# Optimization experiments

Hardware: AMD Instinct MI355X
Metric: run time of the kernel (lower is better)

The kernel has to match this reference:

```python
import jax, jax.numpy as jnp
import numpy as np

D = 1024
NH = 16
HD = D // NH          # 64
GRID = 24             # sqrt(N) for 2D RoPE
HID = 4 * D           # SwiGLU hidden
SOFT_CAP = 50.0
EPS = 1e-6


def _rms(x, g):
    return x * jax.lax.rsqrt(jnp.mean(x * x, axis=-1, keepdims=True) + EPS) * g


def _rotate_half(x):
    h = x.shape[-1] // 2
    return jnp.concatenate([-x[..., h:], x[..., :h]], axis=-1)


def _rope2d_tables():
    half = HD // 2                                   # 32 dims per build, tiled to 64
    inv_freq = 1.0 / (10000.0 ** (jnp.arange(0, half, 2, dtype=jnp.float32) / half))  # (16,)
    idx = jnp.arange(GRID * GRID)
    pr = (idx // GRID).astype(jnp.float32)
    pc = (idx % GRID).astype(jnp.float32)
    freqs = jnp.concatenate([pr[:, None] * inv_freq, pc[:, None] * inv_freq], axis=-1)  # (N,32)
    cos = jnp.concatenate([jnp.cos(freqs), jnp.cos(freqs)], axis=-1)  # (N,64)
    sin = jnp.concatenate([jnp.sin(freqs), jnp.sin(freqs)], axis=-1)
    return cos, sin


def setup_inputs() -> dict:
    key = jax.random.key(0)
    ks = jax.random.split(key, 14)
    B, T, N = 1, 16, GRID * GRID
    s = 0.02
    return {
        "x": jax.random.normal(ks[0], (B, T, N, D), jnp.float32),
        "wq": jax.random.normal(ks[1], (D, D), jnp.float32) * s,
        "wk": jax.random.normal(ks[2], (D, D), jnp.float32) * s,
        "wv": jax.random.normal(ks[3], (D, D), jnp.float32) * s,
        "wo": jax.random.normal(ks[4], (D, D), jnp.float32) * s,
        "gq": jnp.ones((HD,), jnp.float32),
        "gk": jnp.ones((HD,), jnp.float32),
        "g1": jnp.ones((D,), jnp.float32),
        "g2": jnp.ones((D,), jnp.float32),
        "w1": jax.random.normal(ks[5], (D, HID), jnp.float32) * s,
        "w3": jax.random.normal(ks[6], (D, HID), jnp.float32) * s,
        "w2": jax.random.normal(ks[7], (HID, D), jnp.float32) * s,
        "space_mask": jnp.ones((N, N), bool),
        "rope_indices": jnp.arange(N, dtype=jnp.int32),
        "T": 16,
    }


def reference(x, wq, wk, wv, wo, gq, gk, g1, g2, w1, w3, w2, space_mask, rope_indices, T):
    B, T_, N, _ = x.shape
    BT = B * T_
    xs = x.reshape(BT, N, D)

    # --- spatial attention with pre-RMSNorm ---
    h = _rms(xs, g1)
    q = (h @ wq).reshape(BT, N, NH, HD).transpose(0, 2, 1, 3)  # (BT,H,N,hd)
    k = (h @ wk).reshape(BT, N, NH, HD).transpose(0, 2, 1, 3)
    v = (h @ wv).reshape(BT, N, NH, HD).transpose(0, 2, 1, 3)

    # QKNorm: RMSNorm over head_dim with learned scale
    q = q * jax.lax.rsqrt(jnp.mean(q * q, axis=-1, keepdims=True) + EPS) * gq
    k = k * jax.lax.rsqrt(jnp.mean(k * k, axis=-1, keepdims=True) + EPS) * gk

    # 2D RoPE gathered by rope_indices, masked by valid (>=0) indices
    cos, sin = _rope2d_tables()
    safe = jnp.clip(rope_indices, 0, None)
    cos_sel = cos[safe][None, None]  # (1,1,N,hd)
    sin_sel = sin[safe][None, None]
    valid = (rope_indices >= 0)[None, None, :, None]
    q = jnp.where(valid, q * cos_sel + _rotate_half(q) * sin_sel, q)
    k = jnp.where(valid, k * cos_sel + _rotate_half(k) * sin_sel, k)

    scale = HD ** -0.5
    attn = jnp.einsum('bhqd,bhkd->bhqk', q, k) * scale
    attn = SOFT_CAP * jnp.tanh(attn / SOFT_CAP)                 # soft cap
    attn = jnp.where(space_mask[None, None], attn, -jnp.inf)
    attn = jax.nn.softmax(attn.astype(jnp.float32), axis=-1).astype(v.dtype)
    out = jnp.einsum('bhqk,bhkd->bhqd', attn, v)
    out = out.transpose(0, 2, 1, 3).reshape(BT, N, D) @ wo
    xs = xs + out

    # --- SwiGLU FFN with pre-RMSNorm ---
    h2 = _rms(xs, g2)
    ff = (jax.nn.silu(h2 @ w1) * (h2 @ w3)) @ w2
    xs = xs + ff

    return xs.reshape(B, T_, N, D)
```

## Files before the change

### kernel.cpp

```cpp
#include <hip/hip_runtime.h>
#include <hip/hip_bf16.h>


#define D_    1024
#define NH_   16
#define HD_   64
#define NT_   576
#define ROWS_ 9216
#define HID_  4096

typedef __attribute__((ext_vector_type(8))) short bf16x8;
typedef __attribute__((ext_vector_type(4))) float f32x4;

__device__ __forceinline__ unsigned short f2bf(float f) {
  union { float f; unsigned int u; } v; v.f = f;
  unsigned int r = v.u + 0x7FFFu + ((v.u >> 16) & 1u);
  return (unsigned short)(r >> 16);
}
__device__ __forceinline__ float bf2f(unsigned short u) {
  union { unsigned int u; float f; } v; v.u = ((unsigned int)u) << 16;
  return v.f;
}

#define MFMA(a, b, c) __builtin_amdgcn_mfma_f32_16x16x32_bf16((a), (b), (c), 0, 0, 0)

#define GLOAD16(gptr, lptr)                                                        \
  __builtin_amdgcn_global_load_lds(                                                \
      (const __attribute__((address_space(1))) void*)(gptr),                       \
      (__attribute__((address_space(3))) void*)(lptr), 16, 0, 0)

__global__ __launch_bounds__(256) void transpose_w(
    const float* __restrict__ W, unsigned short* __restrict__ Wt, int K, int N) {
  __shared__ float tile[64][65];
  int n0 = blockIdx.x * 64, k0 = blockIdx.y * 64;
  int t = threadIdx.x, c = t & 63, r0 = t >> 6;
#pragma unroll
  for (int i = 0; i < 16; ++i) {
    int r = r0 + i * 4;
    tile[r][c] = W[(size_t)(k0 + r) * N + n0 + c];
  }
  __syncthreads();
#pragma unroll
  for (int i = 0; i < 16; ++i) {
    int r = r0 + i * 4;
    Wt[(size_t)(n0 + r) * K + k0 + c] = f2bf(tile[c][r]);
  }
}

__global__ void rope_tables(float* __restrict__ cosT, float* __restrict__ sinT) {
  int n = blockIdx.x, d = threadIdx.x;
  float pr = (float)(n / 24), pc = (float)(n % 24);
  int fi = d & 31, j = fi & 15;
  float pos = (fi < 16) ? pr : pc;
  float invf = powf(10000.0f, -(float)j * (1.0f / 16.0f));
  float f = pos * invf;
  cosT[n * 64 + d] = cosf(f);
  sinT[n * 64 + d] = sinf(f);
}

__global__ __launch_bounds__(256) void rmsnorm_bf16(
    const float* __restrict__ X, const float* __restrict__ g,
    unsigned short* __restrict__ O) {
  int row = blockIdx.x, t = threadIdx.x;
  const float4 v = ((const float4*)(X + (size_t)row * D_))[t];
  float ss = v.x * v.x + v.y * v.y + v.z * v.z + v.w * v.w;
#pragma unroll
  for (int o = 32; o; o >>= 1) ss += __shfl_xor(ss, o);
  __shared__ float red[4];
  if ((t & 63) == 0) red[t >> 6] = ss;
  __syncthreads();
  float tot = red[0] + red[1] + red[2] + red[3];
  float r = rsqrtf(tot * (1.0f / D_) + 1e-6f);
  const float4 gv = ((const float4*)g)[t];
  ushort4 pack = make_ushort4(f2bf(v.x * r * gv.x), f2bf(v.y * r * gv.y),
                              f2bf(v.z * r * gv.z), f2bf(v.w * r * gv.w));
  ((ushort4*)(O + (size_t)row * D_))[t] = pack;
}

template <int MODE, int BN>
__global__ __launch_bounds__(256) void gemm_bf16(
    const unsigned short* __restrict__ A, const unsigned short* __restrict__ Bt,
    void* __restrict__ Cout, const float* __restrict__ R,
    unsigned short* __restrict__ q_out, unsigned short* __restrict__ k_out,
    unsigned short* __restrict__ v_out, int M, int N, int K) {
  constexpr int NREP = BN / 32;
  __shared__ unsigned short lA[128 * 32];
  __shared__ unsigned short lB[BN * 32];
  const int t = threadIdx.x;
  const int w = t >> 6, l = t & 63;
  const int fr = l & 15, fq = l >> 4;
  const int m0 = blockIdx.y * 128, n0 = blockIdx.x * BN;
  const int wm = (w >> 1) * 64, wn = (w & 1) * (BN / 2);

  f32x4 acc[4][NREP] = {};

  for (int k0 = 0; k0 < K; k0 += 32) {
#pragma unroll
    for (int c = 0; c < 2; ++c) {
      int f = t * 16 + c * 4096;
      GLOAD16(A + (size_t)(m0 + (f >> 6)) * K + k0 + ((f & 63) >> 1),
              (char*)lA + f);
    }
#pragma unroll
    for (int c = 0; c < BN / 64; ++c) {
      int f = t * 16 + c * 4096;
      GLOAD16(Bt + (size_t)(n0 + (f >> 6)) * K + k0 + ((f & 63) >> 1),
              (char*)lB + f);
    }
    __syncthreads();
    bf16x8 af[4], bfr[NREP];
#pragma unroll
    for (int i = 0; i < 4; ++i)
      af[i] = *(const bf16x8*)&lA[(wm + i * 16 + fr) * 32 + fq * 8];
#pragma unroll
    for (int j = 0; j < NREP; ++j)
      bfr[j] = *(const bf16x8*)&lB[(wn + j * 16 + fr) * 32 + fq * 8];
#pragma unroll
    for (int i = 0; i < 4; ++i)
#pragma unroll
      for (int j = 0; j < NREP; ++j)
        acc[i][j] = MFMA(af[i], bfr[j], acc[i][j]);
    __syncthreads();
  }

#pragma unroll
  for (int i = 0; i < 4; ++i)
#pragma unroll
    for (int j = 0; j < NREP; ++j)
#pragma unroll
      for (int e = 0; e < 4; ++e) {
        int rr = m0 + wm + i * 16 + fq * 4 + e;
        int cc = n0 + wn + j * 16 + fr;
        float v = acc[i][j][e];
        if (MODE == 2) {
          size_t idx = (size_t)rr * N + cc;
          ((float*)Cout)[idx] = v + R[idx];
        } else {
          int bt = rr / NT_, n = rr - bt * NT_;
          int part = cc >> 10, cp = cc & 1023;
          int h = cp >> 6, d = cp & 63;
          size_t dst = ((size_t)(bt * NH_ + h) * NT_ + n) * HD_ + d;
          unsigned short bv = f2bf(v);
          if (part == 0) q_out[dst] = bv;
          else if (part == 1) k_out[dst] = bv;
          else v_out[dst] = bv;
        }
      }
}

__global__ __launch_bounds__(256) void gemm_swiglu(
    const unsigned short* __restrict__ A, const unsigned short* __restrict__ B1t,
    const unsigned short* __restrict__ B3t, unsigned short* __restrict__ G,
    int M, int N, int K) {
  __shared__ unsigned short lA[128 * 32];
  __shared__ unsigned short lB1[64 * 32];
  __shared__ unsigned short lB3[64 * 32];
  const int t = threadIdx.x;
  const int w = t >> 6, l = t & 63;
  const int fr = l & 15, fq = l >> 4;
  const int m0 = blockIdx.y * 128, n0 = blockIdx.x * 64;
  const int wm = (w >> 1) * 64, wn = (w & 1) * 32;

  f32x4 a1[4][2] = {}, a3[4][2] = {};

  for (int k0 = 0; k0 < K; k0 += 32) {
#pragma unroll
    for (int c = 0; c < 2; ++c) {
      int f = t * 16 + c * 4096;
      GLOAD16(A + (size_t)(m0 + (f >> 6)) * K + k0 + ((f & 63) >> 1),
              (char*)lA + f);
    }
    {
      int f = t * 16;
      GLOAD16(B1t + (size_t)(n0 + (f >> 6)) * K + k0 + ((f & 63) >> 1),
              (char*)lB1 + f);
      GLOAD16(B3t + (size_t)(n0 + (f >> 6)) * K + k0 + ((f & 63) >> 1),
              (char*)lB3 + f);
    }
    __syncthreads();
    bf16x8 af[4], b1f[2], b3f[2];
#pragma unroll
    for (int i = 0; i < 4; ++i)
      af[i] = *(const bf16x8*)&lA[(wm + i * 16 + fr) * 32 + fq * 8];
#pragma unroll
    for (int j = 0; j < 2; ++j) {
      b1f[j] = *(const bf16x8*)&lB1[(wn + j * 16 + fr) * 32 + fq * 8];
      b3f[j] = *(const bf16x8*)&lB3[(wn + j * 16 + fr) * 32 + fq * 8];
    }
#pragma unroll
    for (int i = 0; i < 4; ++i)
#pragma unroll
      for (int j = 0; j < 2; ++j) {
        a1[i][j] = MFMA(af[i], b1f[j], a1[i][j]);
        a3[i][j] = MFMA(af[i], b3f[j], a3[i][j]);
      }
    __syncthreads();
  }

#pragma unroll
  for (int i = 0; i < 4; ++i)
#pragma unroll
    for (int j = 0; j < 2; ++j)
#pragma unroll
      for (int e = 0; e < 4; ++e) {
        int rr = m0 + wm + i * 16 + fq * 4 + e;
        int cc = n0 + wn + j * 16 + fr;
        float v1 = a1[i][j][e], v3 = a3[i][j][e];
        float s = v1 / (1.0f + __expf(-v1));
        G[(size_t)rr * N + cc] = f2bf(s * v3);
      }
}

__global__ __launch_bounds__(256) void qknorm_rope(
    unsigned short* __restrict__ qh, unsigned short* __restrict__ kh,
    const float* __restrict__ gq, const float* __restrict__ gk,
    const float* __restrict__ cosT, const float* __restrict__ sinT,
    const int* __restrict__ ridx) {
  int gid = blockIdx.x * 4 + (threadIdx.x >> 6);
  int l = threadIdx.x & 63;
  int n = gid % NT_;
  int idx = ridx[n];
  int safe = idx > 0 ? idx : 0;
  float cs = cosT[safe * HD_ + l], sn = sinT[safe * HD_ + l];
  float sign = (l < 32) ? -1.0f : 1.0f;

  size_t base = (size_t)gid * HD_ + l;
  float q = bf2f(qh[base]);
  float k = bf2f(kh[base]);
  float sq = q * q, sk = k * k;
#pragma unroll
  for (int o = 32; o; o >>= 1) {
    sq += __shfl_xor(sq, o);
    sk += __shfl_xor(sk, o);
  }
  float qn = q * rsqrtf(sq * (1.0f / 64) + 1e-6f) * gq[l];
  float kn = k * rsqrtf(sk * (1.0f / 64) + 1e-6f) * gk[l];
  float qp = __shfl_xor(qn, 32), kp = __shfl_xor(kn, 32);
  float qr = qn * cs + sign * qp * sn;
  float kr = kn * cs + sign * kp * sn;
  if (idx < 0) { qr = qn; kr = kn; }
  qh[base] = f2bf(qr);
  kh[base] = f2bf(kr);
}

__global__ __launch_bounds__(256) void v_transpose(
    const unsigned short* __restrict__ vraw, unsigned short* __restrict__ vt) {
  __shared__ unsigned short tile[64][66];
  int n0 = blockIdx.x * 64;
  int bth = blockIdx.y;
  int t = threadIdx.x, c = t & 63, r0 = t >> 6;
#pragma unroll
  for (int i = 0; i < 16; ++i) {
    int r = r0 + i * 4;
    tile[r][c] = vraw[((size_t)bth * NT_ + n0 + r) * HD_ + c];
  }
  __syncthreads();
#pragma unroll
  for (int i = 0; i < 16; ++i) {
    int d = r0 + i * 4;
    vt[((size_t)bth * HD_ + d) * NT_ + n0 + c] = tile[c][d];
  }
}

__global__ __launch_bounds__(256, 4) void attention(
    const unsigned short* __restrict__ qh, const unsigned short* __restrict__ kh,
    const unsigned short* __restrict__ vt, unsigned short* __restrict__ ao) {
  __shared__ unsigned short sQ[16 * 64];
  __shared__ unsigned short sP[16 * 584];
  __shared__ float sRedM[4][16];
  __shared__ float sRedS[4][16];

  const int bid = blockIdx.x;
  const int swz = (bid & 7) * 1152 + (bid >> 3);
  const int bth = swz / 36;
  const int q0 = (swz % 36) * 16;
  const int bt = bth >> 4, h = bth & 15;
  const int t = threadIdx.x, w = t >> 6, l = t & 63;
  const int fr = l & 15, fq = l >> 4;

  if (t < 128)
    GLOAD16(qh + ((size_t)bth * NT_ + q0) * HD_ + t * 8, (char*)sQ + t * 16);
  __syncthreads();

  bf16x8 aq0 = *(const bf16x8*)&sQ[fr * 64 + fq * 8];
  bf16x8 aq1 = *(const bf16x8*)&sQ[fr * 64 + 32 + fq * 8];

  const unsigned short* kb = kh + (size_t)bth * NT_ * HD_;
  f32x4 s[9];
#pragma unroll
  for (int ct = 0; ct < 9; ++ct) {
    int n0 = w * 144 + ct * 16;
    f32x4 acc = {};
    bf16x8 b0 = *(const bf16x8*)(kb + (size_t)(n0 + fr) * HD_ + fq * 8);
    bf16x8 b1 = *(const bf16x8*)(kb + (size_t)(n0 + fr) * HD_ + 32 + fq * 8);
    acc = MFMA(aq0, b0, acc);
    s[ct] = MFMA(aq1, b1, acc);
  }
#pragma unroll
  for (int ct = 0; ct < 9; ++ct)
#pragma unroll
    for (int e = 0; e < 4; ++e) {
      float y2 = s[ct][e] * (2.0f * 0.125f / 50.0f);
      float ex = __expf(y2);
      s[ct][e] = 50.0f - 100.0f / (ex + 1.0f);
    }

  float m[4];
#pragma unroll
  for (int e = 0; e < 4; ++e) {
    float mx = s[0][e];
#pragma unroll
    for (int ct = 1; ct < 9; ++ct) mx = fmaxf(mx, s[ct][e]);
#pragma unroll
    for (int o = 1; o < 16; o <<= 1) mx = fmaxf(mx, __shfl_xor(mx, o));
    m[e] = mx;
  }
  if (fr == 0)
#pragma unroll
    for (int e = 0; e < 4; ++e) sRedM[w][fq * 4 + e] = m[e];
  __syncthreads();
#pragma unroll
  for (int e = 0; e < 4; ++e) {
    int rq = fq * 4 + e;
    m[e] = fmaxf(fmaxf(sRedM[0][rq], sRedM[1][rq]),
                 fmaxf(sRedM[2][rq], sRedM[3][rq]));
  }

  float sum[4];
#pragma unroll
  for (int e = 0; e < 4; ++e) {
    float sm = 0.f;
#pragma unroll
    for (int ct = 0; ct < 9; ++ct) {
      float pv = __expf(s[ct][e] - m[e]);
      s[ct][e] = pv;
      sm += pv;
    }
#pragma unroll
    for (int o = 1; o < 16; o <<= 1) sm += __shfl_xor(sm, o);
    sum[e] = sm;
  }
  if (fr == 0)
#pragma unroll
    for (int e = 0; e < 4; ++e) sRedS[w][fq * 4 + e] = sum[e];
  __syncthreads();

#pragma unroll
  for (int e = 0; e < 4; ++e) {
    int rq = fq * 4 + e;
    float inv = 1.0f / (sRedS[0][rq] + sRedS[1][rq] +
                        sRedS[2][rq] + sRedS[3][rq]);
#pragma unroll
    for (int ct = 0; ct < 9; ++ct)
      sP[rq * 584 + w * 144 + ct * 16 + fr] = f2bf(s[ct][e] * inv);
  }
  __syncthreads();

  const int c0 = w * 16;
  const unsigned short* vb = vt + (size_t)bth * HD_ * NT_;
  f32x4 oa = {};
#pragma unroll
  for (int ks = 0; ks < 18; ++ks) {
    bf16x8 ap = *(const bf16x8*)&sP[fr * 584 + ks * 32 + fq * 8];
    bf16x8 bv = *(const bf16x8*)(vb + (size_t)(c0 + fr) * NT_ + ks * 32 + fq * 8);
    oa = MFMA(ap, bv, oa);
  }
#pragma unroll
  for (int e = 0; e < 4; ++e) {
    int rq = fq * 4 + e;
    ao[((size_t)(bt * NT_ + q0 + rq)) * D_ + h * HD_ + c0 + fr] = f2bf(oa[e]);
  }
}

extern "C" void kernel_launch(void* const* d_in, const int* in_sizes, int n_in,
                              void* d_out, int out_size, void* d_ws, size_t ws_size,
                              hipStream_t stream) {
  const float* x  = (const float*)d_in[0];
  const float* wq = (const float*)d_in[1];
  const float* wk = (const float*)d_in[2];
  const float* wv = (const float*)d_in[3];
  const float* wo = (const float*)d_in[4];
  const float* gq = (const float*)d_in[5];
  const float* gk = (const float*)d_in[6];
  const float* g1 = (const float*)d_in[7];
  const float* g2 = (const float*)d_in[8];
  const float* w1 = (const float*)d_in[9];
  const float* w3 = (const float*)d_in[10];
  const float* w2 = (const float*)d_in[11];
  const int* ridx = (const int*)d_in[13];

  char* p = (char*)d_ws;
  unsigned short* wqkvT = (unsigned short*)(p);
  unsigned short* woT   = (unsigned short*)(p + 6291456);
  unsigned short* w1T   = (unsigned short*)(p + 8388608);
  unsigned short* w3T   = (unsigned short*)(p + 16777216);
  unsigned short* w2T   = (unsigned short*)(p + 25165824);
  float* cosT = (float*)(p + 33554432);
  float* sinT = (float*)(p + 33701888);
  unsigned short* hb = (unsigned short*)(p + 33849344);
  char* big = p + 52723712;
  unsigned short* qh   = (unsigned short*)(big);
  unsigned short* kh   = (unsigned short*)(big + 18874368);
  unsigned short* vraw = (unsigned short*)(big + 37748736);
  unsigned short* vt   = (unsigned short*)(big + 56623104);
  unsigned short* ao   = vraw;
  unsigned short* gbuf = (unsigned short*)(big);
  float* xs1 = (float*)d_out;

  transpose_w<<<dim3(16, 16), 256, 0, stream>>>(wq, wqkvT,               1024, 1024);
  transpose_w<<<dim3(16, 16), 256, 0, stream>>>(wk, wqkvT + 1024 * 1024, 1024, 1024);
  transpose_w<<<dim3(16, 16), 256, 0, stream>>>(wv, wqkvT + 2048 * 1024, 1024, 1024);
  transpose_w<<<dim3(16, 16), 256, 0, stream>>>(wo, woT,                 1024, 1024);
  transpose_w<<<dim3(64, 16), 256, 0, stream>>>(w1, w1T, 1024, 4096);
  transpose_w<<<dim3(64, 16), 256, 0, stream>>>(w3, w3T, 1024, 4096);
  transpose_w<<<dim3(16, 64), 256, 0, stream>>>(w2, w2T, 4096, 1024);
  rope_tables<<<576, 64, 0, stream>>>(cosT, sinT);

  rmsnorm_bf16<<<ROWS_, 256, 0, stream>>>(x, g1, hb);
  gemm_bf16<4, 128><<<dim3(24, 72), 256, 0, stream>>>(hb, wqkvT, nullptr, nullptr,
                                                      qh, kh, vraw, ROWS_, 3072, 1024);
  qknorm_rope<<<36864, 256, 0, stream>>>(qh, kh, gq, gk, cosT, sinT, ridx);
  v_transpose<<<dim3(9, 256), 256, 0, stream>>>(vraw, vt);
  attention<<<9216, 256, 0, stream>>>(qh, kh, vt, ao);
  gemm_bf16<2, 128><<<dim3(8, 72), 256, 0, stream>>>(ao, woT, xs1, x,
                                                     nullptr, nullptr, nullptr,
                                                     ROWS_, 1024, 1024);

  rmsnorm_bf16<<<ROWS_, 256, 0, stream>>>(xs1, g2, hb);
  gemm_swiglu<<<dim3(64, 72), 256, 0, stream>>>(hb, w1T, w3T, gbuf,
                                                ROWS_, HID_, 1024);
  gemm_bf16<2, 64><<<dim3(16, 72), 256, 0, stream>>>(gbuf, w2T, (float*)d_out, xs1,
                                                     nullptr, nullptr, nullptr,
                                                     ROWS_, 1024, HID_);
}
```

Before: 861.8 us.

## Triple-buffer GEMM LDS stages with vmcnt waits and shrink QKV/O tiles

```diff
diff --git a/kernel.cpp b/kernel.cpp
--- a/kernel.cpp
+++ b/kernel.cpp
@@ -28,6 +28,13 @@
   __builtin_amdgcn_global_load_lds(                                                \
       (const __attribute__((address_space(1))) void*)(gptr),                       \
       (__attribute__((address_space(3))) void*)(lptr), 16, 0, 0)
+
+#define VMCNT(N) asm volatile("s_waitcnt vmcnt(" #N ")" ::: "memory")
+#define PIPE_BARRIER()                         \
+  do {                                         \
+    __builtin_amdgcn_s_barrier();              \
+    __builtin_amdgcn_sched_barrier(0);         \
+  } while (0)
 
 __global__ __launch_bounds__(256) void transpose_w(
     const float* __restrict__ W, unsigned short* __restrict__ Wt, int K, int N) {
@@ -84,8 +91,9 @@
     unsigned short* __restrict__ q_out, unsigned short* __restrict__ k_out,
     unsigned short* __restrict__ v_out, int M, int N, int K) {
   constexpr int NREP = BN / 32;
-  __shared__ unsigned short lA[128 * 32];
-  __shared__ unsigned short lB[BN * 32];
+  constexpr int BOPS = BN / 64;
+  __shared__ unsigned short lA[3][128 * 32];
+  __shared__ unsigned short lB[3][BN * 32];
   const int t = threadIdx.x;
   const int w = t >> 6, l = t & 63;
   const int fr = l & 15, fq = l >> 4;
@@ -94,33 +102,54 @@
 
   f32x4 acc[4][NREP] = {};
 
-  for (int k0 = 0; k0 < K; k0 += 32) {
+  auto STAGE = [&](int s, int k0) {
 #pragma unroll
     for (int c = 0; c < 2; ++c) {
       int f = t * 16 + c * 4096;
       GLOAD16(A + (size_t)(m0 + (f >> 6)) * K + k0 + ((f & 63) >> 1),
-              (char*)lA + f);
-    }
-#pragma unroll
-    for (int c = 0; c < BN / 64; ++c) {
+              (char*)lA[s] + f);
+    }
+#pragma unroll
+    for (int c = 0; c < BOPS; ++c) {
       int f = t * 16 + c * 4096;
       GLOAD16(Bt + (size_t)(n0 + (f >> 6)) * K + k0 + ((f & 63) >> 1),
-              (char*)lB + f);
-    }
-    __syncthreads();
+              (char*)lB[s] + f);
+    }
+  };
+
+  const int NK = K >> 5;
+  STAGE(0, 0);
+  STAGE(1, 32);
+  if constexpr (BOPS == 2) VMCNT(4); else VMCNT(3);
+  PIPE_BARRIER();
+
+  int slot = 0;
+  for (int kt = 0; kt < NK; ++kt) {
+    if (kt + 2 < NK) {
+      int s2 = slot + 2; if (s2 >= 3) s2 -= 3;
+      STAGE(s2, (kt + 2) << 5);
+    }
     bf16x8 af[4], bfr[NREP];
 #pragma unroll
     for (int i = 0; i < 4; ++i)
-      af[i] = *(const bf16x8*)&lA[(wm + i * 16 + fr) * 32 + fq * 8];
+      af[i] = *(const bf16x8*)&lA[slot][(wm + i * 16 + fr) * 32 + fq * 8];
 #pragma unroll
     for (int j = 0; j < NREP; ++j)
-      bfr[j] = *(const bf16x8*)&lB[(wn + j * 16 + fr) * 32 + fq * 8];
+      bfr[j] = *(const bf16x8*)&lB[slot][(wn + j * 16 + fr) * 32 + fq * 8];
+    __builtin_amdgcn_s_setprio(1);
 #pragma unroll
     for (int i = 0; i < 4; ++i)
 #pragma unroll
       for (int j = 0; j < NREP; ++j)
         acc[i][j] = MFMA(af[i], bfr[j], acc[i][j]);
-    __syncthreads();
+    __builtin_amdgcn_s_setprio(0);
+    if (kt + 2 < NK) {
+      if constexpr (BOPS == 2) VMCNT(4); else VMCNT(3);
+    } else if (kt + 1 < NK) {
+      VMCNT(0);
+    }
+    PIPE_BARRIER();
+    ++slot; if (slot == 3) slot = 0;
   }
 
 #pragma unroll
@@ -152,9 +181,9 @@
     const unsigned short* __restrict__ A, const unsigned short* __restrict__ B1t,
     const unsigned short* __restrict__ B3t, unsigned short* __restrict__ G,
     int M, int N, int K) {
-  __shared__ unsigned short lA[128 * 32];
-  __shared__ unsigned short lB1[64 * 32];
-  __shared__ unsigned short lB3[64 * 32];
+  __shared__ unsigned short lA[3][128 * 32];
+  __shared__ unsigned short lB1[3][64 * 32];
+  __shared__ unsigned short lB3[3][64 * 32];
   const int t = threadIdx.x;
   const int w = t >> 6, l = t & 63;
   const int fr = l & 15, fq = l >> 4;
@@ -163,30 +192,42 @@
 
   f32x4 a1[4][2] = {}, a3[4][2] = {};
 
-  for (int k0 = 0; k0 < K; k0 += 32) {
+  auto STAGE = [&](int s, int k0) {
 #pragma unroll
     for (int c = 0; c < 2; ++c) {
       int f = t * 16 + c * 4096;
       GLOAD16(A + (size_t)(m0 + (f >> 6)) * K + k0 + ((f & 63) >> 1),
-              (char*)lA + f);
-    }
-    {
-      int f = t * 16;
-      GLOAD16(B1t + (size_t)(n0 + (f >> 6)) * K + k0 + ((f & 63) >> 1),
-              (char*)lB1 + f);
-      GLOAD16(B3t + (size_t)(n0 + (f >> 6)) * K + k0 + ((f & 63) >> 1),
-              (char*)lB3 + f);
-    }
-    __syncthreads();
+              (char*)lA[s] + f);
+    }
+    int f = t * 16;
+    GLOAD16(B1t + (size_t)(n0 + (f >> 6)) * K + k0 + ((f & 63) >> 1),
+            (char*)lB1[s] + f);
+    GLOAD16(B3t + (size_t)(n0 + (f >> 6)) * K + k0 + ((f & 63) >> 1),
+            (char*)lB3[s] + f);
+  };
+
+  const int NK = K >> 5;
+  STAGE(0, 0);
+  STAGE(1, 32);
+  VMCNT(4);
+  PIPE_BARRIER();
+
+  int slot = 0;
+  for (int kt = 0; kt < NK; ++kt) {
+    if (kt + 2 < NK) {
+      int s2 = slot + 2; if (s2 >= 3) s2 -= 3;
+      STAGE(s2, (kt + 2) << 5);
+    }
     bf16x8 af[4], b1f[2], b3f[2];
 #pragma unroll
     for (int i = 0; i < 4; ++i)
-      af[i] = *(const bf16x8*)&lA[(wm + i * 16 + fr) * 32 + fq * 8];
+      af[i] = *(const bf16x8*)&lA[slot][(wm + i * 16 + fr) * 32 + fq * 8];
 #pragma unroll
     for (int j = 0; j < 2; ++j) {
-      b1f[j] = *(const bf16x8*)&lB1[(wn + j * 16 + fr) * 32 + fq * 8];
-      b3f[j] = *(const bf16x8*)&lB3[(wn + j * 16 + fr) * 32 + fq * 8];
-    }
+      b1f[j] = *(const bf16x8*)&lB1[slot][(wn + j * 16 + fr) * 32 + fq * 8];
+      b3f[j] = *(const bf16x8*)&lB3[slot][(wn + j * 16 + fr) * 32 + fq * 8];
+    }
+    __builtin_amdgcn_s_setprio(1);
 #pragma unroll
     for (int i = 0; i < 4; ++i)
 #pragma unroll
@@ -194,7 +235,11 @@
         a1[i][j] = MFMA(af[i], b1f[j], a1[i][j]);
         a3[i][j] = MFMA(af[i], b3f[j], a3[i][j]);
       }
-    __syncthreads();
+    __builtin_amdgcn_s_setprio(0);
+    if (kt + 2 < NK) VMCNT(4);
+    else if (kt + 1 < NK) VMCNT(0);
+    PIPE_BARRIER();
+    ++slot; if (slot == 3) slot = 0;
   }
 
 #pragma unroll
@@ -417,12 +462,12 @@
   rope_tables<<<576, 64, 0, stream>>>(cosT, sinT);
 
   rmsnorm_bf16<<<ROWS_, 256, 0, stream>>>(x, g1, hb);
-  gemm_bf16<4, 128><<<dim3(24, 72), 256, 0, stream>>>(hb, wqkvT, nullptr, nullptr,
-                                                      qh, kh, vraw, ROWS_, 3072, 1024);
+  gemm_bf16<4, 64><<<dim3(48, 72), 256, 0, stream>>>(hb, wqkvT, nullptr, nullptr,
+                                                     qh, kh, vraw, ROWS_, 3072, 1024);
   qknorm_rope<<<36864, 256, 0, stream>>>(qh, kh, gq, gk, cosT, sinT, ridx);
   v_transpose<<<dim3(9, 256), 256, 0, stream>>>(vraw, vt);
   attention<<<9216, 256, 0, stream>>>(qh, kh, vt, ao);
-  gemm_bf16<2, 128><<<dim3(8, 72), 256, 0, stream>>>(ao, woT, xs1, x,
+  gemm_bf16<2, 64><<<dim3(16, 72), 256, 0, stream>>>(ao, woT, xs1, x,
                                                      nullptr, nullptr, nullptr,
                                                      ROWS_, 1024, 1024);
 
```

Measured after the change: 850.3 us. About the same (-1.3%).
